# Kernel tuning notes

Measured on AMD Instinct MI355X. Metric: run time of the kernel, lower is better.

The kernel has to match this reference:

```python
import jax, jax.numpy as jnp
import numpy as np

DIM = 1024
H = 8
HK = DIM // H  # head key dim = 128 (expand_k=1.0)
HV = DIM // H  # head value dim = 128 (expand_v=1.0)
GLR = 16       # gate low-rank dim (fla default)
GATE_LOGIT_NORMALIZER = 16.0
EPS = 1e-5
B, T = 2, 512


def setup_inputs() -> dict:
    key = jax.random.key(0)
    ks = jax.random.split(key, 9)
    s = lambda k, shp: jax.random.normal(k, shp, jnp.float32) * (shp[0] ** -0.5)
    return {
        "x": jax.random.normal(ks[0], (B, T, DIM), jnp.float32),
        "Wq": s(ks[1], (DIM, DIM)),
        "Wk": s(ks[2], (DIM, DIM)),
        "Wv": s(ks[3], (DIM, DIM)),
        "Wg": s(ks[4], (DIM, DIM)),
        "Wgk1": s(ks[5], (DIM, GLR)),
        "Wgk2": s(ks[6], (GLR, DIM)),
        "bgk2": jnp.zeros((DIM,), jnp.float32),
        "g_norm_w": jnp.ones((HV,), jnp.float32),
        "Wo": s(ks[7], (DIM, DIM)),
    }


def _gla_forward(x, Wq, Wk, Wv, Wg, Wgk1, Wgk2, bgk2, g_norm_w, Wo):
    b, t, _ = x.shape
    # projections
    q = (x @ Wq).reshape(b, t, H, HK) * (HK ** -0.5)
    k = (x @ Wk).reshape(b, t, H, HK)
    v = (x @ Wv).reshape(b, t, H, HV)
    # low-rank forget gate: logsigmoid / normalizer, per key channel
    gk = (jax.nn.log_sigmoid((x @ Wgk1) @ Wgk2 + bgk2) / GATE_LOGIT_NORMALIZER)
    gk = gk.reshape(b, t, H, HK)

    # recurrent decay-gated linear attention:
    #   S_t = diag(exp(gk_t)) @ S_{t-1} + k_t^T v_t ; o_t = q_t @ S_t
    def step(h, inp):
        qt, kt, vt, gt = inp  # each [B, H, HK] / [B, H, HV]
        h = h * jnp.exp(gt)[..., None] + kt[..., None] * vt[..., None, :]
        ot = jnp.einsum("bhk,bhkv->bhv", qt, h)
        return h, ot

    h0 = jnp.zeros((b, H, HK, HV), x.dtype)
    xs = (
        q.transpose(1, 0, 2, 3),
        k.transpose(1, 0, 2, 3),
        v.transpose(1, 0, 2, 3),
        gk.transpose(1, 0, 2, 3),
    )
    _, o = jax.lax.scan(step, h0, xs)  # o: [T, B, H, HV]
    o = o.transpose(1, 0, 2, 3)        # [B, T, H, HV]

    # gated RMSNorm with swish gate over per-head value dim, then output proj
    g = (x @ Wg).reshape(b, t, H, HV)
    rms = jax.lax.rsqrt(jnp.mean(o * o, axis=-1, keepdims=True) + EPS)
    o = (o * rms) * g_norm_w * (g * jax.nn.sigmoid(g))
    return o.reshape(b, t, DIM) @ Wo


def reference(x, Wq, Wk, Wv, Wg, Wgk1, Wgk2, bgk2, g_norm_w, Wo):
    return _gla_forward(x, Wq, Wk, Wv, Wg, Wgk1, Wgk2, bgk2, g_norm_w, Wo)
```

## Files before the change

### kernel.cpp

```cpp
#include <hip/hip_runtime.h>
#include <hip/hip_bf16.h>
#include <math.h>

#define BT     1024
#define NH     8
#define SEGLEN 32
#define NSEG   16
#define NBH    16
#define QKS    136
#define VTS    40
#define AMS    40

typedef __attribute__((ext_vector_type(8))) short short8;
typedef __attribute__((ext_vector_type(4))) short sh4;
typedef __attribute__((ext_vector_type(4))) float f32x4;

__device__ __forceinline__ float bitf(short u) {
    union { float f; unsigned i; } x; x.i = ((unsigned)(unsigned short)u) << 16; return x.f;
}
__device__ __forceinline__ short f2bf(float f) {
    union { float f; unsigned u; } x; x.f = f;
    unsigned r = x.u + 0x7FFF + ((x.u >> 16) & 1);
    return (short)(r >> 16);
}
__device__ __forceinline__ void gload_lds16(const short* g, short* l) {
    __builtin_amdgcn_global_load_lds(
        (const __attribute__((address_space(1))) unsigned int*)g,
        (__attribute__((address_space(3))) unsigned int*)l, 16, 0, 0);
}

__global__ __launch_bounds__(256) void cast_all(
    const float* __restrict__ Wq, const float* __restrict__ Wk,
    const float* __restrict__ Wv, const float* __restrict__ Wg,
    const float* __restrict__ Wo, const float* __restrict__ X,
    short* __restrict__ WT, short* __restrict__ Xb)
{
    const int z = blockIdx.z;
    const int tid = threadIdx.x;
    if (z == 5) {
        const int id = blockIdx.y * 32 + blockIdx.x;
        const int i = id * 1024 + tid * 4;
        float4 a = *(const float4*)(X + i);
        sh4 v;
        v[0] = f2bf(a.x); v[1] = f2bf(a.y); v[2] = f2bf(a.z); v[3] = f2bf(a.w);
        *(sh4*)(Xb + i) = v;
        return;
    }
    const float* W = (z == 0) ? Wq : (z == 1) ? Wk : (z == 2) ? Wv : (z == 3) ? Wg : Wo;
    short* T = WT + (size_t)z * (1u << 20);
    __shared__ float tile[32][33];
    const int k0 = blockIdx.y * 32, n0 = blockIdx.x * 32;
    const int row = tid >> 3, c4 = (tid & 7) << 2;
    float4 f = *(const float4*)(W + (size_t)(k0 + row) * 1024 + n0 + c4);
    tile[row][c4 + 0] = f.x; tile[row][c4 + 1] = f.y;
    tile[row][c4 + 2] = f.z; tile[row][c4 + 3] = f.w;
    __syncthreads();
    short* o = T + (size_t)(n0 + row) * 1024 + k0 + c4;
    o[0] = f2bf(tile[c4 + 0][row]); o[1] = f2bf(tile[c4 + 1][row]);
    o[2] = f2bf(tile[c4 + 2][row]); o[3] = f2bf(tile[c4 + 3][row]);
}

__global__ __launch_bounds__(256) void proj_gemm(
    const short* __restrict__ Xb, const short* __restrict__ WT,
    short* __restrict__ QKVG)
{
    const int z = blockIdx.z;
    const float scale = (z == 0) ? 0.08838834764831845f : 1.0f;
    short* C = QKVG + (size_t)z * (1u << 20);
    const short* B = WT + (size_t)z * (1u << 20);

    __shared__ __align__(16) short As[8 * 64 * 8];
    __shared__ __align__(16) short Bs[8 * 64 * 8];
    const int tid = threadIdx.x;
    const int wave = tid >> 6, lane = tid & 63;
    const int wm = (wave >> 1) * 32, wn = (wave & 1) * 32;
    const int m15 = lane & 15, q = lane >> 4;
    const int m0 = blockIdx.y * 64, n0 = blockIdx.x * 64;

    f32x4 acc[2][2];
    #pragma unroll
    for (int i = 0; i < 2; i++)
        #pragma unroll
        for (int j = 0; j < 2; j++)
            acc[i][j] = (f32x4){0.f, 0.f, 0.f, 0.f};

    for (int kb0 = 0; kb0 < 1024; kb0 += 64) {
        __syncthreads();
        #pragma unroll
        for (int c = 0; c < 2; c++) {
            const int k8 = wave * 2 + c;
            gload_lds16(Xb + (size_t)(m0 + lane) * 1024 + kb0 + k8 * 8, &As[(k8 * 64) * 8]);
            gload_lds16(B  + (size_t)(n0 + lane) * 1024 + kb0 + k8 * 8, &Bs[(k8 * 64) * 8]);
        }
        __syncthreads();
        #pragma unroll
        for (int s = 0; s < 2; s++) {
            const int k8 = s * 4 + q;
            short8 af[2], bf[2];
            #pragma unroll
            for (int i = 0; i < 2; i++)
                af[i] = *(const short8*)&As[(k8 * 64 + wm + i * 16 + m15) * 8];
            #pragma unroll
            for (int j = 0; j < 2; j++)
                bf[j] = *(const short8*)&Bs[(k8 * 64 + wn + j * 16 + m15) * 8];
            #pragma unroll
            for (int i = 0; i < 2; i++)
                #pragma unroll
                for (int j = 0; j < 2; j++)
                    acc[i][j] = __builtin_amdgcn_mfma_f32_16x16x32_bf16(af[i], bf[j], acc[i][j], 0, 0, 0);
        }
    }
    #pragma unroll
    for (int i = 0; i < 2; i++)
        #pragma unroll
        for (int j = 0; j < 2; j++)
            #pragma unroll
            for (int rr = 0; rr < 4; rr++)
                C[(size_t)(m0 + wm + i * 16 + q * 4 + rr) * 1024 + n0 + wn + j * 16 + m15] =
                    f2bf(acc[i][j][rr] * scale);
}

__global__ __launch_bounds__(256) void wo_gemm(
    const short* __restrict__ A, const short* __restrict__ B, float* __restrict__ C)
{
    __shared__ __align__(16) short As[8 * 64 * 8];
    __shared__ __align__(16) short Bs[8 * 64 * 8];
    const int tid = threadIdx.x;
    const int wave = tid >> 6, lane = tid & 63;
    const int wm = (wave >> 1) * 32, wn = (wave & 1) * 32;
    const int m15 = lane & 15, q = lane >> 4;
    const int m0 = blockIdx.y * 64, n0 = blockIdx.x * 64;

    f32x4 acc[2][2];
    #pragma unroll
    for (int i = 0; i < 2; i++)
        #pragma unroll
        for (int j = 0; j < 2; j++)
            acc[i][j] = (f32x4){0.f, 0.f, 0.f, 0.f};

    for (int kb0 = 0; kb0 < 1024; kb0 += 64) {
        __syncthreads();
        #pragma unroll
        for (int c = 0; c < 2; c++) {
            const int k8 = wave * 2 + c;
            gload_lds16(A + (size_t)(m0 + lane) * 1024 + kb0 + k8 * 8, &As[(k8 * 64) * 8]);
            gload_lds16(B + (size_t)(n0 + lane) * 1024 + kb0 + k8 * 8, &Bs[(k8 * 64) * 8]);
        }
        __syncthreads();
        #pragma unroll
        for (int s = 0; s < 2; s++) {
            const int k8 = s * 4 + q;
            short8 af[2], bf[2];
            #pragma unroll
            for (int i = 0; i < 2; i++)
                af[i] = *(const short8*)&As[(k8 * 64 + wm + i * 16 + m15) * 8];
            #pragma unroll
            for (int j = 0; j < 2; j++)
                bf[j] = *(const short8*)&Bs[(k8 * 64 + wn + j * 16 + m15) * 8];
            #pragma unroll
            for (int i = 0; i < 2; i++)
                #pragma unroll
                for (int j = 0; j < 2; j++)
                    acc[i][j] = __builtin_amdgcn_mfma_f32_16x16x32_bf16(af[i], bf[j], acc[i][j], 0, 0, 0);
        }
    }
    #pragma unroll
    for (int i = 0; i < 2; i++)
        #pragma unroll
        for (int j = 0; j < 2; j++)
            #pragma unroll
            for (int rr = 0; rr < 4; rr++)
                C[(size_t)(m0 + wm + i * 16 + q * 4 + rr) * 1024 + n0 + wn + j * 16 + m15] =
                    acc[i][j][rr];
}

__global__ __launch_bounds__(256) void gk_proj(
    const short* __restrict__ Xb, const float* __restrict__ Wgk1,
    const float* __restrict__ Wgk2, const float* __restrict__ bgk2,
    short* __restrict__ GK)
{
    const int row = blockIdx.x, tid = threadIdx.x;
    float p[16];
    #pragma unroll
    for (int j = 0; j < 16; j++) p[j] = 0.f;
    for (int d = tid; d < 1024; d += 256) {
        float xv = bitf(Xb[(size_t)row * 1024 + d]);
        #pragma unroll
        for (int j = 0; j < 16; j++)
            p[j] = fmaf(xv, Wgk1[d * 16 + j], p[j]);
    }
    #pragma unroll
    for (int j = 0; j < 16; j++)
        for (int off = 32; off; off >>= 1) p[j] += __shfl_down(p[j], off);
    __shared__ float zp[4][16];
    __shared__ float z[16];
    const int lane = tid & 63, w = tid >> 6;
    if (lane == 0) {
        #pragma unroll
        for (int j = 0; j < 16; j++) zp[w][j] = p[j];
    }
    __syncthreads();
    if (tid < 16) z[tid] = zp[0][tid] + zp[1][tid] + zp[2][tid] + zp[3][tid];
    __syncthreads();
    for (int c = tid; c < 1024; c += 256) {
        float acc = bgk2[c];
        #pragma unroll
        for (int j = 0; j < 16; j++)
            acc = fmaf(z[j], Wgk2[j * 1024 + c], acc);
        float ls = fminf(acc, 0.f) - log1pf(expf(-fabsf(acc)));
        GK[(size_t)row * 1024 + c] = f2bf(ls * (1.f / 16.f));
    }
}

__global__ __launch_bounds__(256) void scan_chunk(
    const short* __restrict__ Q, const short* __restrict__ K,
    const short* __restrict__ V, short* GKQT,
    float* __restrict__ O, short* __restrict__ SS, float* __restrict__ DSEG)
{
    const int seg = blockIdx.x;
    const int bh  = blockIdx.y;
    const int b = bh >> 3, h = bh & 7;
    const int tid = threadIdx.x;
    const size_t rowbase = (size_t)(b * 512 + seg * SEGLEN) * 1024 + h * 128;

    __shared__ __align__(16) short Qt[32 * QKS];
    __shared__ __align__(16) short Kt[32 * QKS];
    __shared__ __align__(16) short Vs[32 * 128];
    __shared__ __align__(16) short VT[128 * VTS];
    __shared__ __align__(16) short KhT[128 * VTS];
    __shared__ __align__(16) short Am[32 * AMS];

    if (tid < 128) {
        const int ch = tid;
        float gsum = 0.f;
        float ktf[32];
        #pragma unroll
        for (int t = 0; t < 32; t++) {
            const size_t a = rowbase + (size_t)t * 1024 + ch;
            float g  = bitf(GKQT[a]);
            float kv = bitf(K[a]);
            float qv = bitf(Q[a]);
            gsum += g;
            float eg  = expf(gsum);
            float emg = expf(-gsum);
            short qts = f2bf(qv * eg);
            Qt[t * QKS + ch] = qts;
            GKQT[a] = qts;
            float ktv = kv * emg;
            Kt[t * QKS + ch] = f2bf(ktv);
            ktf[t] = ktv;
        }
        float eGend = expf(gsum);
        DSEG[(bh * NSEG + seg) * 128 + ch] = eGend;
        #pragma unroll
        for (int t4 = 0; t4 < 8; t4++) {
            sh4 p;
            p[0] = f2bf(ktf[4 * t4 + 0] * eGend);
            p[1] = f2bf(ktf[4 * t4 + 1] * eGend);
            p[2] = f2bf(ktf[4 * t4 + 2] * eGend);
            p[3] = f2bf(ktf[4 * t4 + 3] * eGend);
            *(sh4*)&KhT[ch * VTS + 4 * t4] = p;
        }
    } else {
        const int u = tid - 128;
        #pragma unroll
        for (int i = 0; i < 4; i++) {
            const int idx = u + i * 128;
            const int t = idx >> 4, c = idx & 15;
            short8 vv = *(const short8*)&V[rowbase + (size_t)t * 1024 + c * 8];
            *(short8*)&Vs[t * 128 + c * 8] = vv;
        }
    }
    __syncthreads();
    {
        const int ch = tid >> 1, t0 = (tid & 1) * 16;
        #pragma unroll
        for (int j = 0; j < 4; j++) {
            sh4 p;
            p[0] = Vs[(t0 + 4 * j + 0) * 128 + ch];
            p[1] = Vs[(t0 + 4 * j + 1) * 128 + ch];
            p[2] = Vs[(t0 + 4 * j + 2) * 128 + ch];
            p[3] = Vs[(t0 + 4 * j + 3) * 128 + ch];
            *(sh4*)&VT[ch * VTS + t0 + 4 * j] = p;
        }
    }
    __syncthreads();

    const int wave = tid >> 6, lane = tid & 63;
    const int m15 = lane & 15, q = lane >> 4;

    {
        const int mi = wave >> 1, ni = wave & 1;
        f32x4 a1 = (f32x4){0.f, 0.f, 0.f, 0.f};
        #pragma unroll
        for (int kc = 0; kc < 4; kc++) {
            short8 af = *(const short8*)&Qt[(mi * 16 + m15) * QKS + kc * 32 + q * 8];
            short8 bf = *(const short8*)&Kt[(ni * 16 + m15) * QKS + kc * 32 + q * 8];
            a1 = __builtin_amdgcn_mfma_f32_16x16x32_bf16(af, bf, a1, 0, 0, 0);
        }
        #pragma unroll
        for (int rr = 0; rr < 4; rr++) {
            const int t = mi * 16 + q * 4 + rr, s = ni * 16 + m15;
            Am[t * AMS + s] = (t >= s) ? f2bf(a1[rr]) : (short)0;
        }
    }
    __syncthreads();

    {
        const int mi = wave >> 1, nb = (wave & 1) * 4;
        short8 af = *(const short8*)&Am[(mi * 16 + m15) * AMS + q * 8];
        #pragma unroll
        for (int jj = 0; jj < 4; jj++) {
            short8 bf = *(const short8*)&VT[((nb + jj) * 16 + m15) * VTS + q * 8];
            f32x4 a2 = (f32x4){0.f, 0.f, 0.f, 0.f};
            a2 = __builtin_amdgcn_mfma_f32_16x16x32_bf16(af, bf, a2, 0, 0, 0);
            #pragma unroll
            for (int rr = 0; rr < 4; rr++)
                O[rowbase + (size_t)(mi * 16 + q * 4 + rr) * 1024 + (nb + jj) * 16 + m15] = a2[rr];
        }
    }

    {
        const size_t sbase = (size_t)(bh * NSEG + seg) * 16384;
        #pragma unroll
        for (int m2 = 0; m2 < 2; m2++) {
            const int mrow = wave * 2 + m2;
            short8 af = *(const short8*)&VT[(mrow * 16 + m15) * VTS + q * 8];
            #pragma unroll
            for (int ni = 0; ni < 8; ni++) {
                short8 bf = *(const short8*)&KhT[(ni * 16 + m15) * VTS + q * 8];
                f32x4 a3 = (f32x4){0.f, 0.f, 0.f, 0.f};
                a3 = __builtin_amdgcn_mfma_f32_16x16x32_bf16(af, bf, a3, 0, 0, 0);
                #pragma unroll
                for (int rr = 0; rr < 4; rr++)
                    SS[sbase + (size_t)(mrow * 16 + q * 4 + rr) * 128 + ni * 16 + m15] =
                        f2bf(a3[rr]);
            }
        }
    }
}

__global__ __launch_bounds__(256) void stitch(
    short* __restrict__ SS, const float* __restrict__ DSEG)
{
    const int slice = blockIdx.x;
    const int bh = blockIdx.y, tid = threadIdx.x;
    __shared__ float dloc[NSEG][128];
    for (int i = tid; i < NSEG * 128; i += 256)
        dloc[i >> 7][i & 127] = DSEG[(bh * NSEG + (i >> 7)) * 128 + (i & 127)];
    __syncthreads();
    const int kch = tid & 127;
    float run[8];
    #pragma unroll
    for (int j = 0; j < 8; j++) run[j] = 0.f;
    for (int seg = 0; seg < NSEG; seg++) {
        const size_t base = (size_t)(bh * NSEG + seg) * 16384 + slice * 2048;
        const float dk = dloc[seg][kch];
        #pragma unroll
        for (int j = 0; j < 8; j++) {
            const int e = j * 256 + tid;
            float tmp = bitf(SS[base + e]);
            SS[base + e] = f2bf(run[j]);
            run[j] = fmaf(run[j], dk, tmp);
        }
    }
}

__global__ __launch_bounds__(256) void corr_gnorm(
    const short* __restrict__ QT, const short* __restrict__ SS,
    const float* __restrict__ O, const short* __restrict__ G,
    const float* __restrict__ gnw, short* __restrict__ Obf)
{
    const int seg = blockIdx.x;
    const int bh = blockIdx.y;
    const int b = bh >> 3, h = bh & 7;
    const int tid = threadIdx.x;
    const int wave = tid >> 6, lane = tid & 63;
    const int m15 = lane & 15, q = lane >> 4;
    const size_t rowbase = (size_t)(b * 512 + seg * SEGLEN) * 1024 + h * 128;
    const size_t sbase = (size_t)(bh * NSEG + seg) * 16384;

    __shared__ __align__(16) short Qs[16 * 32 * 8];
    __shared__ __align__(16) short Ss[16 * 128 * 8];
    __shared__ float red[4][16];

    #pragma unroll
    for (int c = 0; c < 2; c++) {
        const int fb = wave * 128 + c * 64;
        const int flat = fb + lane;
        const int k8 = flat >> 5, t = flat & 31;
        gload_lds16(QT + rowbase + (size_t)t * 1024 + k8 * 8, &Qs[fb * 8]);
    }
    #pragma unroll
    for (int c = 0; c < 8; c++) {
        const int fb = wave * 512 + c * 64;
        const int flat = fb + lane;
        const int k8 = flat >> 7, vch = flat & 127;
        gload_lds16(SS + sbase + (size_t)vch * 128 + k8 * 8, &Ss[fb * 8]);
    }
    __syncthreads();

    const int mt = wave >> 1, nh2 = wave & 1;
    f32x4 acc[4];
    #pragma unroll
    for (int nt = 0; nt < 4; nt++) acc[nt] = (f32x4){0.f, 0.f, 0.f, 0.f};
    #pragma unroll
    for (int kb = 0; kb < 4; kb++) {
        short8 af = *(const short8*)&Qs[((kb * 4 + q) * 32 + mt * 16 + m15) * 8];
        #pragma unroll
        for (int nt = 0; nt < 4; nt++) {
            short8 bf = *(const short8*)&Ss[((kb * 4 + q) * 128 + nh2 * 64 + nt * 16 + m15) * 8];
            acc[nt] = __builtin_amdgcn_mfma_f32_16x16x32_bf16(af, bf, acc[nt], 0, 0, 0);
        }
    }

    float o[4][4];
    float ssq[4] = {0.f, 0.f, 0.f, 0.f};
    #pragma unroll
    for (int nt = 0; nt < 4; nt++) {
        const int vch = nh2 * 64 + nt * 16 + m15;
        #pragma unroll
        for (int rr = 0; rr < 4; rr++) {
            const int t = mt * 16 + q * 4 + rr;
            float ov = O[rowbase + (size_t)t * 1024 + vch] + acc[nt][rr];
            o[nt][rr] = ov;
            ssq[rr] = fmaf(ov, ov, ssq[rr]);
        }
    }
    #pragma unroll
    for (int rr = 0; rr < 4; rr++) {
        ssq[rr] += __shfl_xor(ssq[rr], 1);
        ssq[rr] += __shfl_xor(ssq[rr], 2);
        ssq[rr] += __shfl_xor(ssq[rr], 4);
        ssq[rr] += __shfl_xor(ssq[rr], 8);
    }
    if (m15 == 0) {
        #pragma unroll
        for (int rr = 0; rr < 4; rr++) red[wave][q * 4 + rr] = ssq[rr];
    }
    __syncthreads();
    float rsq[4];
    #pragma unroll
    for (int rr = 0; rr < 4; rr++) {
        float ms = (red[wave][q * 4 + rr] + red[wave ^ 1][q * 4 + rr]) * (1.f / 128.f);
        rsq[rr] = rsqrtf(ms + 1e-5f);
    }
    #pragma unroll
    for (int nt = 0; nt < 4; nt++) {
        const int vch = nh2 * 64 + nt * 16 + m15;
        const float gw = gnw[vch];
        #pragma unroll
        for (int rr = 0; rr < 4; rr++) {
            const int t = mt * 16 + q * 4 + rr;
            float g = bitf(G[rowbase + (size_t)t * 1024 + vch]);
            float sg = g / (1.f + expf(-g));
            Obf[rowbase + (size_t)t * 1024 + vch] = f2bf(o[nt][rr] * rsq[rr] * gw * sg);
        }
    }
}

extern "C" void kernel_launch(void* const* d_in, const int* in_sizes, int n_in,
                              void* d_out, int out_size, void* d_ws, size_t ws_size,
                              hipStream_t stream)
{
    const float* X    = (const float*)d_in[0];
    const float* Wq   = (const float*)d_in[1];
    const float* Wk   = (const float*)d_in[2];
    const float* Wv   = (const float*)d_in[3];
    const float* Wg   = (const float*)d_in[4];
    const float* Wgk1 = (const float*)d_in[5];
    const float* Wgk2 = (const float*)d_in[6];
    const float* bgk2 = (const float*)d_in[7];
    const float* gnw  = (const float*)d_in[8];
    const float* Wo   = (const float*)d_in[9];
    float* OUT = (float*)d_out;

    short* QKVG = (short*)d_ws;
    short* GK   = QKVG + (4u << 20);
    float* Ob   = (float*)(GK + (1u << 20));
    short* SS   = (short*)(Ob + (1u << 20));
    float* DS   = (float*)(SS + (4u << 20));
    short* WT   = (short*)(DS + 32768);
    short* Xb   = WT + (5u << 20);
    short* Obf  = QKVG;

    cast_all<<<dim3(32, 32, 6), 256, 0, stream>>>(Wq, Wk, Wv, Wg, Wo, X, WT, Xb);
    proj_gemm<<<dim3(16, 16, 4), 256, 0, stream>>>(Xb, WT, QKVG);
    gk_proj<<<dim3(BT), 256, 0, stream>>>(Xb, Wgk1, Wgk2, bgk2, GK);
    scan_chunk<<<dim3(NSEG, NBH), 256, 0, stream>>>(
        QKVG, QKVG + (1u << 20), QKVG + (2u << 20), GK, Ob, SS, DS);
    stitch<<<dim3(8, NBH), 256, 0, stream>>>(SS, DS);
    corr_gnorm<<<dim3(NSEG, NBH), 256, 0, stream>>>(
        GK, SS, Ob, QKVG + (3u << 20), gnw, Obf);
    wo_gemm<<<dim3(16, 16), 256, 0, stream>>>(Obf, WT + (4u << 20), OUT);
}
```

Baseline: 175.3 us.

## Fuse gate low-rank projection into projection GEMM and tune scan pipeline stages

Folds the gk low-rank gate computation into the projection GEMM launch as an extra z-slice, one wave per row, which removes a kernel launch and its 1024-block grid. The intra-chunk output O is now stored as bf16 rather than fp32, halving that intermediate traffic at some cost in precision. The scan kernel splits the cumulative gate sum across both thread halves and loads V asynchronously into LDS. The stitch kernel gets twice as many blocks and uses paired bf16 accesses. corr_gnorm stages G and O through LDS with async loads instead of scattered global reads.

```diff
diff --git a/kernel.cpp b/kernel.cpp
--- a/kernel.cpp
+++ b/kernel.cpp
@@ -60,15 +60,101 @@
     o[2] = f2bf(tile[c4 + 2][row]); o[3] = f2bf(tile[c4 + 3][row]);
 }
 
-__global__ __launch_bounds__(256) void proj_gemm(
+__global__ __launch_bounds__(256) void proj_gk(
     const short* __restrict__ Xb, const short* __restrict__ WT,
-    short* __restrict__ QKVG)
+    short* __restrict__ QKVG,
+    const float* __restrict__ Wgk1, const float* __restrict__ Wgk2,
+    const float* __restrict__ bgk2, short* __restrict__ GK)
 {
     const int z = blockIdx.z;
+    const int tid = threadIdx.x;
+    const int wave = tid >> 6, lane = tid & 63;
+
+    if (z == 4) {
+        const int row = (blockIdx.y * 16 + blockIdx.x) * 4 + wave;
+        float p[16];
+        #pragma unroll
+        for (int j = 0; j < 16; j++) p[j] = 0.f;
+        for (int d8 = 0; d8 < 16; d8++) {
+            const int d = d8 * 64 + lane;
+            float xv = bitf(Xb[(size_t)row * 1024 + d]);
+            #pragma unroll
+            for (int j = 0; j < 16; j++)
+                p[j] = fmaf(xv, Wgk1[d * 16 + j], p[j]);
+        }
+        #pragma unroll
+        for (int j = 0; j < 16; j++)
+            #pragma unroll
+            for (int off = 32; off; off >>= 1)
+                p[j] += __shfl_xor(p[j], off);
+        for (int c8 = 0; c8 < 16; c8++) {
+            const int c = c8 * 64 + lane;
+            float acc = bgk2[c];
+            #pragma unroll
+            for (int j = 0; j < 16; j++)
+                acc = fmaf(p[j], Wgk2[j * 1024 + c], acc);
+            float ls = fminf(acc, 0.f) - log1pf(expf(-fabsf(acc)));
+            GK[(size_t)row * 1024 + c] = f2bf(ls * (1.f / 16.f));
+        }
+        return;
+    }
+
     const float scale = (z == 0) ? 0.08838834764831845f : 1.0f;
     short* C = QKVG + (size_t)z * (1u << 20);
     const short* B = WT + (size_t)z * (1u << 20);
 
+    __shared__ __align__(16) short As[8 * 64 * 8];
+    __shared__ __align__(16) short Bs[8 * 64 * 8];
+    const int wm = (wave >> 1) * 32, wn = (wave & 1) * 32;
+    const int m15 = lane & 15, q = lane >> 4;
+    const int m0 = blockIdx.y * 64, n0 = blockIdx.x * 64;
+
+    f32x4 acc[2][2];
+    #pragma unroll
+    for (int i = 0; i < 2; i++)
+        #pragma unroll
+        for (int j = 0; j < 2; j++)
+            acc[i][j] = (f32x4){0.f, 0.f, 0.f, 0.f};
+
+    for (int kb0 = 0; kb0 < 1024; kb0 += 64) {
+        __syncthreads();
+        #pragma unroll
+        for (int c = 0; c < 2; c++) {
+            const int k8 = wave * 2 + c;
+            gload_lds16(Xb + (size_t)(m0 + lane) * 1024 + kb0 + k8 * 8, &As[(k8 * 64) * 8]);
+            gload_lds16(B  + (size_t)(n0 + lane) * 1024 + kb0 + k8 * 8, &Bs[(k8 * 64) * 8]);
+        }
+        __syncthreads();
+        #pragma unroll
+        for (int s = 0; s < 2; s++) {
+            const int k8 = s * 4 + q;
+            short8 af[2], bf[2];
+            #pragma unroll
+            for (int i = 0; i < 2; i++)
+                af[i] = *(const short8*)&As[(k8 * 64 + wm + i * 16 + m15) * 8];
+            #pragma unroll
+            for (int j = 0; j < 2; j++)
+                bf[j] = *(const short8*)&Bs[(k8 * 64 + wn + j * 16 + m15) * 8];
+            #pragma unroll
+            for (int i = 0; i < 2; i++)
+                #pragma unroll
+                for (int j = 0; j < 2; j++)
+                    acc[i][j] = __builtin_amdgcn_mfma_f32_16x16x32_bf16(af[i], bf[j], acc[i][j], 0, 0, 0);
+        }
+    }
+    #pragma unroll
+    for (int i = 0; i < 2; i++)
+        #pragma unroll
+        for (int j = 0; j < 2; j++)
+            #pragma unroll
+            for (int rr = 0; rr < 4; rr++)
+                C[(size_t)(m0 + wm + i * 16 + q * 4 + rr) * 1024 + n0 + wn + j * 16 + m15] =
+                    f2bf(acc[i][j][rr] * scale);
+}
+
+__global__ __launch_bounds__(256) void wo_gemm(
+    const short* __restrict__ A, const short* __restrict__ B, float* __restrict__ C)
+{
     __shared__ __align__(16) short As[8 * 64 * 8];
     __shared__ __align__(16) short Bs[8 * 64 * 8];
     const int tid = threadIdx.x;
@@ -89,8 +175,8 @@
         #pragma unroll
         for (int c = 0; c < 2; c++) {
             const int k8 = wave * 2 + c;
-            gload_lds16(Xb + (size_t)(m0 + lane) * 1024 + kb0 + k8 * 8, &As[(k8 * 64) * 8]);
-            gload_lds16(B  + (size_t)(n0 + lane) * 1024 + kb0 + k8 * 8, &Bs[(k8 * 64) * 8]);
+            gload_lds16(A + (size_t)(m0 + lane) * 1024 + kb0 + k8 * 8, &As[(k8 * 64) * 8]);
+            gload_lds16(B + (size_t)(n0 + lane) * 1024 + kb0 + k8 * 8, &Bs[(k8 * 64) * 8]);
         }
         __syncthreads();
         #pragma unroll
@@ -117,110 +203,19 @@
             #pragma unroll
             for (int rr = 0; rr < 4; rr++)
                 C[(size_t)(m0 + wm + i * 16 + q * 4 + rr) * 1024 + n0 + wn + j * 16 + m15] =
-                    f2bf(acc[i][j][rr] * scale);
-}
-
-__global__ __launch_bounds__(256) void wo_gemm(
-    const short* __restrict__ A, const short* __restrict__ B, float* __restrict__ C)
-{
-    __shared__ __align__(16) short As[8 * 64 * 8];
-    __shared__ __align__(16) short Bs[8 * 64 * 8];
-    const int tid = threadIdx.x;
-    const int wave = tid >> 6, lane = tid & 63;
-    const int wm = (wave >> 1) * 32, wn = (wave & 1) * 32;
-    const int m15 = lane & 15, q = lane >> 4;
-    const int m0 = blockIdx.y * 64, n0 = blockIdx.x * 64;
-
-    f32x4 acc[2][2];
-    #pragma unroll
-    for (int i = 0; i < 2; i++)
-        #pragma unroll
-        for (int j = 0; j < 2; j++)
-            acc[i][j] = (f32x4){0.f, 0.f, 0.f, 0.f};
-
-    for (int kb0 = 0; kb0 < 1024; kb0 += 64) {
-        __syncthreads();
-        #pragma unroll
-        for (int c = 0; c < 2; c++) {
-            const int k8 = wave * 2 + c;
-            gload_lds16(A + (size_t)(m0 + lane) * 1024 + kb0 + k8 * 8, &As[(k8 * 64) * 8]);
-            gload_lds16(B + (size_t)(n0 + lane) * 1024 + kb0 + k8 * 8, &Bs[(k8 * 64) * 8]);
-        }
-        __syncthreads();
-        #pragma unroll
-        for (int s = 0; s < 2; s++) {
-            const int k8 = s * 4 + q;
-            short8 af[2], bf[2];
-            #pragma unroll
-            for (int i = 0; i < 2; i++)
-                af[i] = *(const short8*)&As[(k8 * 64 + wm + i * 16 + m15) * 8];
-            #pragma unroll
-            for (int j = 0; j < 2; j++)
-                bf[j] = *(const short8*)&Bs[(k8 * 64 + wn + j * 16 + m15) * 8];
-            #pragma unroll
-            for (int i = 0; i < 2; i++)
-                #pragma unroll
-                for (int j = 0; j < 2; j++)
-                    acc[i][j] = __builtin_amdgcn_mfma_f32_16x16x32_bf16(af[i], bf[j], acc[i][j], 0, 0, 0);
-        }
-    }
-    #pragma unroll
-    for (int i = 0; i < 2; i++)
-        #pragma unroll
-        for (int j = 0; j < 2; j++)
-            #pragma unroll
-            for (int rr = 0; rr < 4; rr++)
-                C[(size_t)(m0 + wm + i * 16 + q * 4 + rr) * 1024 + n0 + wn + j * 16 + m15] =
                     acc[i][j][rr];
-}
-
-__global__ __launch_bounds__(256) void gk_proj(
-    const short* __restrict__ Xb, const float* __restrict__ Wgk1,
-    const float* __restrict__ Wgk2, const float* __restrict__ bgk2,
-    short* __restrict__ GK)
-{
-    const int row = blockIdx.x, tid = threadIdx.x;
-    float p[16];
-    #pragma unroll
-    for (int j = 0; j < 16; j++) p[j] = 0.f;
-    for (int d = tid; d < 1024; d += 256) {
-        float xv = bitf(Xb[(size_t)row * 1024 + d]);
-        #pragma unroll
-        for (int j = 0; j < 16; j++)
-            p[j] = fmaf(xv, Wgk1[d * 16 + j], p[j]);
-    }
-    #pragma unroll
-    for (int j = 0; j < 16; j++)
-        for (int off = 32; off; off >>= 1) p[j] += __shfl_down(p[j], off);
-    __shared__ float zp[4][16];
-    __shared__ float z[16];
-    const int lane = tid & 63, w = tid >> 6;
-    if (lane == 0) {
-        #pragma unroll
-        for (int j = 0; j < 16; j++) zp[w][j] = p[j];
-    }
-    __syncthreads();
-    if (tid < 16) z[tid] = zp[0][tid] + zp[1][tid] + zp[2][tid] + zp[3][tid];
-    __syncthreads();
-    for (int c = tid; c < 1024; c += 256) {
-        float acc = bgk2[c];
-        #pragma unroll
-        for (int j = 0; j < 16; j++)
-            acc = fmaf(z[j], Wgk2[j * 1024 + c], acc);
-        float ls = fminf(acc, 0.f) - log1pf(expf(-fabsf(acc)));
-        GK[(size_t)row * 1024 + c] = f2bf(ls * (1.f / 16.f));
-    }
 }
 
 __global__ __launch_bounds__(256) void scan_chunk(
     const short* __restrict__ Q, const short* __restrict__ K,
     const short* __restrict__ V, short* GKQT,
-    float* __restrict__ O, short* __restrict__ SS, float* __restrict__ DSEG)
+    short* __restrict__ O, short* __restrict__ SS, float* __restrict__ DSEG)
 {
     const int seg = blockIdx.x;
     const int bh  = blockIdx.y;
     const int b = bh >> 3, h = bh & 7;
     const int tid = threadIdx.x;
+    const int wave = tid >> 6, lane = tid & 63;
     const size_t rowbase = (size_t)(b * 512 + seg * SEGLEN) * 1024 + h * 128;
 
     __shared__ __align__(16) short Qt[32 * QKS];
@@ -229,64 +224,59 @@
     __shared__ __align__(16) short VT[128 * VTS];
     __shared__ __align__(16) short KhT[128 * VTS];
     __shared__ __align__(16) short Am[32 * AMS];
-
-    if (tid < 128) {
-        const int ch = tid;
-        float gsum = 0.f;
-        float ktf[32];
-        #pragma unroll
-        for (int t = 0; t < 32; t++) {
-            const size_t a = rowbase + (size_t)t * 1024 + ch;
-            float g  = bitf(GKQT[a]);
-            float kv = bitf(K[a]);
-            float qv = bitf(Q[a]);
-            gsum += g;
-            float eg  = expf(gsum);
-            float emg = expf(-gsum);
-            short qts = f2bf(qv * eg);
-            Qt[t * QKS + ch] = qts;
-            GKQT[a] = qts;
-            float ktv = kv * emg;
-            Kt[t * QKS + ch] = f2bf(ktv);
-            ktf[t] = ktv;
-        }
-        float eGend = expf(gsum);
-        DSEG[(bh * NSEG + seg) * 128 + ch] = eGend;
-        #pragma unroll
-        for (int t4 = 0; t4 < 8; t4++) {
-            sh4 p;
-            p[0] = f2bf(ktf[4 * t4 + 0] * eGend);
-            p[1] = f2bf(ktf[4 * t4 + 1] * eGend);
-            p[2] = f2bf(ktf[4 * t4 + 2] * eGend);
-            p[3] = f2bf(ktf[4 * t4 + 3] * eGend);
-            *(sh4*)&KhT[ch * VTS + 4 * t4] = p;
-        }
-    } else {
-        const int u = tid - 128;
-        #pragma unroll
-        for (int i = 0; i < 4; i++) {
-            const int idx = u + i * 128;
-            const int t = idx >> 4, c = idx & 15;
-            short8 vv = *(const short8*)&V[rowbase + (size_t)t * 1024 + c * 8];
-            *(short8*)&Vs[t * 128 + c * 8] = vv;
-        }
+    __shared__ float htot[2][128];
+
+    #pragma unroll
+    for (int c = 0; c < 2; c++) {
+        const int fb = (wave * 2 + c) * 64;
+        const int f = fb + lane;
+        const int t = f >> 4, c8 = f & 15;
+        gload_lds16(V + rowbase + (size_t)t * 1024 + c8 * 8, &Vs[fb * 8]);
+    }
+
+    const int ch = tid & 127, th2 = tid >> 7;
+    float g[16], kv[16], qv[16];
+    #pragma unroll
+    for (int tt = 0; tt < 16; tt++) {
+        const size_t a = rowbase + (size_t)(th2 * 16 + tt) * 1024 + ch;
+        g[tt] = bitf(GKQT[a]); kv[tt] = bitf(K[a]); qv[tt] = bitf(Q[a]);
+    }
+    float run = 0.f;
+    #pragma unroll
+    for (int tt = 0; tt < 16; tt++) { run += g[tt]; g[tt] = run; }
+    htot[th2][ch] = run;
+    __syncthreads();
+    const float base_ = th2 ? htot[0][ch] : 0.f;
+    const float eGend = expf(htot[0][ch] + htot[1][ch]);
+    if (th2 == 0) DSEG[(bh * NSEG + seg) * 128 + ch] = eGend;
+    #pragma unroll
+    for (int tt = 0; tt < 16; tt++) {
+        const int t = th2 * 16 + tt;
+        const size_t a = rowbase + (size_t)t * 1024 + ch;
+        const float Gc = base_ + g[tt];
+        const float eg = expf(Gc);
+        short qts = f2bf(qv[tt] * eg);
+        Qt[t * QKS + ch] = qts;
+        GKQT[a] = qts;
+        float ktv = kv[tt] * expf(-Gc);
+        Kt[t * QKS + ch] = f2bf(ktv);
+        KhT[ch * VTS + t] = f2bf(ktv * eGend);
     }
     __syncthreads();
     {
-        const int ch = tid >> 1, t0 = (tid & 1) * 16;
+        const int vch = tid >> 1, t0 = (tid & 1) * 16;
         #pragma unroll
         for (int j = 0; j < 4; j++) {
             sh4 p;
-            p[0] = Vs[(t0 + 4 * j + 0) * 128 + ch];
-            p[1] = Vs[(t0 + 4 * j + 1) * 128 + ch];
-            p[2] = Vs[(t0 + 4 * j + 2) * 128 + ch];
-            p[3] = Vs[(t0 + 4 * j + 3) * 128 + ch];
-            *(sh4*)&VT[ch * VTS + t0 + 4 * j] = p;
-        }
-    }
-    __syncthreads();
-
-    const int wave = tid >> 6, lane = tid & 63;
+            p[0] = Vs[(t0 + 4 * j + 0) * 128 + vch];
+            p[1] = Vs[(t0 + 4 * j + 1) * 128 + vch];
+            p[2] = Vs[(t0 + 4 * j + 2) * 128 + vch];
+            p[3] = Vs[(t0 + 4 * j + 3) * 128 + vch];
+            *(sh4*)&VT[vch * VTS + t0 + 4 * j] = p;
+        }
+    }
+    __syncthreads();
+
     const int m15 = lane & 15, q = lane >> 4;
 
     {
@@ -316,7 +306,8 @@
             a2 = __builtin_amdgcn_mfma_f32_16x16x32_bf16(af, bf, a2, 0, 0, 0);
             #pragma unroll
             for (int rr = 0; rr < 4; rr++)
-                O[rowbase + (size_t)(mi * 16 + q * 4 + rr) * 1024 + (nb + jj) * 16 + m15] = a2[rr];
+                O[rowbase + (size_t)(mi * 16 + q * 4 + rr) * 1024 + (nb + jj) * 16 + m15] =
+                    f2bf(a2[rr]);
         }
     }
 
@@ -349,26 +340,29 @@
     for (int i = tid; i < NSEG * 128; i += 256)
         dloc[i >> 7][i & 127] = DSEG[(bh * NSEG + (i >> 7)) * 128 + (i & 127)];
     __syncthreads();
-    const int kch = tid & 127;
-    float run[8];
-    #pragma unroll
-    for (int j = 0; j < 8; j++) run[j] = 0.f;
+    const int kch0 = (tid * 2) & 127;
+    float run[2][2] = {{0.f, 0.f}, {0.f, 0.f}};
     for (int seg = 0; seg < NSEG; seg++) {
-        const size_t base = (size_t)(bh * NSEG + seg) * 16384 + slice * 2048;
-        const float dk = dloc[seg][kch];
-        #pragma unroll
-        for (int j = 0; j < 8; j++) {
-            const int e = j * 256 + tid;
-            float tmp = bitf(SS[base + e]);
-            SS[base + e] = f2bf(run[j]);
-            run[j] = fmaf(run[j], dk, tmp);
+        const size_t base = (size_t)(bh * NSEG + seg) * 16384 + slice * 1024;
+        const float d0 = dloc[seg][kch0], d1 = dloc[seg][kch0 + 1];
+        #pragma unroll
+        for (int j = 0; j < 2; j++) {
+            unsigned* p = (unsigned*)&SS[base + j * 512 + tid * 2];
+            unsigned u = *p;
+            float t0 = bitf((short)(u & 0xFFFF));
+            float t1 = bitf((short)(u >> 16));
+            unsigned w0 = (unsigned short)f2bf(run[j][0]);
+            unsigned w1 = (unsigned short)f2bf(run[j][1]);
+            *p = w0 | (w1 << 16);
+            run[j][0] = fmaf(run[j][0], d0, t0);
+            run[j][1] = fmaf(run[j][1], d1, t1);
         }
     }
 }
 
 __global__ __launch_bounds__(256) void corr_gnorm(
     const short* __restrict__ QT, const short* __restrict__ SS,
-    const float* __restrict__ O, const short* __restrict__ G,
+    const short* __restrict__ O, const short* __restrict__ G,
     const float* __restrict__ gnw, short* __restrict__ Obf)
 {
     const int seg = blockIdx.x;
@@ -382,20 +376,30 @@
 
     __shared__ __align__(16) short Qs[16 * 32 * 8];
     __shared__ __align__(16) short Ss[16 * 128 * 8];
+    __shared__ __align__(16) short Gs[16 * 32 * 8];
+    __shared__ __align__(16) short Os[16 * 32 * 8];
     __shared__ float red[4][16];
 
     #pragma unroll
     for (int c = 0; c < 2; c++) {
-        const int fb = wave * 128 + c * 64;
-        const int flat = fb + lane;
-        const int k8 = flat >> 5, t = flat & 31;
+        const int fb = (wave * 2 + c) * 64;
+        const int f = fb + lane;
+        const int k8 = f >> 5, t = f & 31;
         gload_lds16(QT + rowbase + (size_t)t * 1024 + k8 * 8, &Qs[fb * 8]);
+    }
+    #pragma unroll
+    for (int c = 0; c < 2; c++) {
+        const int fb = (wave * 2 + c) * 64;
+        const int f = fb + lane;
+        const int v8 = f >> 5, t = f & 31;
+        gload_lds16(G + rowbase + (size_t)t * 1024 + v8 * 8, &Gs[fb * 8]);
+        gload_lds16(O + rowbase + (size_t)t * 1024 + v8 * 8, &Os[fb * 8]);
     }
     #pragma unroll
     for (int c = 0; c < 8; c++) {
         const int fb = wave * 512 + c * 64;
-        const int flat = fb + lane;
-        const int k8 = flat >> 7, vch = flat & 127;
+        const int f = fb + lane;
+        const int k8 = f >> 7, vch = f & 127;
         gload_lds16(SS + sbase + (size_t)vch * 128 + k8 * 8, &Ss[fb * 8]);
     }
     __syncthreads();
@@ -422,7 +426,7 @@
         #pragma unroll
         for (int rr = 0; rr < 4; rr++) {
             const int t = mt * 16 + q * 4 + rr;
-            float ov = O[rowbase + (size_t)t * 1024 + vch] + acc[nt][rr];
+            float ov = bitf(Os[((vch >> 3) * 32 + t) * 8 + (vch & 7)]) + acc[nt][rr];
             o[nt][rr] = ov;
             ssq[rr] = fmaf(ov, ov, ssq[rr]);
         }
@@ -452,7 +456,7 @@
         #pragma unroll
         for (int rr = 0; rr < 4; rr++) {
             const int t = mt * 16 + q * 4 + rr;
-            float g = bitf(G[rowbase + (size_t)t * 1024 + vch]);
+            float g = bitf(Gs[((vch >> 3) * 32 + t) * 8 + (vch & 7)]);
             float sg = g / (1.f + expf(-g));
             Obf[rowbase + (size_t)t * 1024 + vch] = f2bf(o[nt][rr] * rsq[rr] * gw * sg);
         }
@@ -477,19 +481,18 @@
 
     short* QKVG = (short*)d_ws;
     short* GK   = QKVG + (4u << 20);
-    float* Ob   = (float*)(GK + (1u << 20));
-    short* SS   = (short*)(Ob + (1u << 20));
+    short* Ob   = GK + (1u << 20);
+    short* SS   = Ob + (1u << 20);
     float* DS   = (float*)(SS + (4u << 20));
     short* WT   = (short*)(DS + 32768);
     short* Xb   = WT + (5u << 20);
     short* Obf  = QKVG;
 
     cast_all<<<dim3(32, 32, 6), 256, 0, stream>>>(Wq, Wk, Wv, Wg, Wo, X, WT, Xb);
-    proj_gemm<<<dim3(16, 16, 4), 256, 0, stream>>>(Xb, WT, QKVG);
-    gk_proj<<<dim3(BT), 256, 0, stream>>>(Xb, Wgk1, Wgk2, bgk2, GK);
+    proj_gk<<<dim3(16, 16, 5), 256, 0, stream>>>(Xb, WT, QKVG, Wgk1, Wgk2, bgk2, GK);
     scan_chunk<<<dim3(NSEG, NBH), 256, 0, stream>>>(
         QKVG, QKVG + (1u << 20), QKVG + (2u << 20), GK, Ob, SS, DS);
-    stitch<<<dim3(8, NBH), 256, 0, stream>>>(SS, DS);
+    stitch<<<dim3(16, NBH), 256, 0, stream>>>(SS, DS);
     corr_gnorm<<<dim3(NSEG, NBH), 256, 0, stream>>>(
         GK, SS, Ob, QKVG + (3u << 20), gnw, Obf);
     wo_gemm<<<dim3(16, 16), 256, 0, stream>>>(Obf, WT + (4u << 20), OUT);
```

After: 174.1 us. About the same (-0.7%).
